# Kernel tuning notes

Measured on AMD Instinct MI355X. Metric: run time of the kernel, lower is better.

Reference implementation:

```python
import jax, jax.numpy as jnp
import numpy as np

N, LAT, HID = 4, 256, 512
OMICS = [("ge", 20000), ("meth", 200000), ("mirna", 2000), ("cnv", 25000)]
EPS = 1e-3  # Keras BatchNormalization default epsilon

# Fully-connected latent graph (i != j) + self loops (added by GCNConv).
_src = np.array([i for i in range(N) for j in range(N) if i != j] + list(range(N)), dtype=np.int32)
_dst = np.array([j for i in range(N) for j in range(N) if i != j] + list(range(N)), dtype=np.int32)
# Every node has degree N (N-1 neighbors + self loop) -> sym norm 1/sqrt(N*N) = 1/N per edge.
_norm = np.full(len(_src), 1.0 / N, dtype=np.float32)


def _gcn(x, W):
    h = x @ W                                   # [N, LAT] transform
    msg = h[_src] * _norm[:, None]              # gather + edge-normalize
    return jax.ops.segment_sum(msg, _dst, num_segments=N)  # scatter-add


def _bn(x, g, b, m, v):
    # BatchNorm in inference mode: moving stats.
    return g * (x - m) * jax.lax.rsqrt(v + EPS) + b


def setup_inputs() -> dict:
    key = jax.random.key(0)
    ks = list(jax.random.split(key, 4 + len(OMICS)))
    d = {
        "latent_vectors": jax.random.normal(ks[0], (N, LAT), jnp.float32),
        "Wg1": jax.random.normal(ks[1], (LAT, LAT), jnp.float32) * 0.05,
        "Wg2": jax.random.normal(ks[2], (LAT, LAT), jnp.float32) * 0.05,
        "W1": jax.random.normal(ks[3], (N, LAT, HID), jnp.float32) * 0.05,
        "b1": jnp.zeros((N, HID), jnp.float32),
        "g1": jnp.ones((N, HID), jnp.float32),
        "be1": jnp.zeros((N, HID), jnp.float32),
        "m1": jnp.zeros((N, HID), jnp.float32),
        "v1": jnp.ones((N, HID), jnp.float32),
    }
    for k, (name, dim) in enumerate(OMICS):
        d[f"W2_{name}"] = jax.random.normal(ks[4 + k], (HID, dim), jnp.float32) * 0.02
        d[f"b2_{name}"] = jnp.zeros((dim,), jnp.float32)
        d[f"g2_{name}"] = jnp.ones((dim,), jnp.float32)
        d[f"be2_{name}"] = jnp.zeros((dim,), jnp.float32)
        d[f"m2_{name}"] = jnp.zeros((dim,), jnp.float32)
        d[f"v2_{name}"] = jnp.ones((dim,), jnp.float32)
    return d


def _forward(latent_vectors, Wg1, Wg2, W1, b1, g1, be1, m1, v1, per_omics):
    # Two GCN layers + ReLU (dropout inactive: training=False)
    x = jax.nn.relu(_gcn(latent_vectors, Wg1))
    x = jax.nn.relu(_gcn(x, Wg2))               # [N, LAT]
    # First dense stage of all generators, vectorized over nodes.
    h = jnp.einsum('td,tdh->th', x, W1) + b1     # [N, HID]
    h = jax.nn.relu(_bn(h, g1, be1, m1, v1))     # BN (inference) + ReLU; dropout off
    outs = []
    for i, (W2, b2, g2, be2, m2, v2) in enumerate(per_omics):
        y = h[i] @ W2 + b2                       # [output_dim_i]
        outs.append(_bn(y, g2, be2, m2, v2))
    return tuple(outs)


def reference(latent_vectors, Wg1, Wg2, W1, b1, g1, be1, m1, v1,
              W2_ge, b2_ge, g2_ge, be2_ge, m2_ge, v2_ge,
              W2_meth, b2_meth, g2_meth, be2_meth, m2_meth, v2_meth,
              W2_mirna, b2_mirna, g2_mirna, be2_mirna, m2_mirna, v2_mirna,
              W2_cnv, b2_cnv, g2_cnv, be2_cnv, m2_cnv, v2_cnv):
    per = [(W2_ge, b2_ge, g2_ge, be2_ge, m2_ge, v2_ge),
           (W2_meth, b2_meth, g2_meth, be2_meth, m2_meth, v2_meth),
           (W2_mirna, b2_mirna, g2_mirna, be2_mirna, m2_mirna, v2_mirna),
           (W2_cnv, b2_cnv, g2_cnv, be2_cnv, m2_cnv, v2_cnv)]
    return _forward(latent_vectors, Wg1, Wg2, W1, b1, g1, be1, m1, v1, per)
```

## Files before the change

### kernel.cpp

```cpp
#include <hip/hip_runtime.h>


#define EPS 1e-3f

typedef unsigned short u16;
typedef unsigned int   u32;

__device__ __forceinline__ float b2f(u16 u) {
    union { u32 i; float f; } v; v.i = ((u32)u) << 16; return v.f;
}
__device__ __forceinline__ float lo16(u32 u) {
    union { u32 i; float f; } v; v.i = u << 16; return v.f;
}
__device__ __forceinline__ float hi16(u32 u) {
    union { u32 i; float f; } v; v.i = u & 0xffff0000u; return v.f;
}
__device__ __forceinline__ u16 f2b(float f) {
    union { float f; u32 i; } v; v.f = f;
    u32 r = v.i + 0x7fffu + ((v.i >> 16) & 1u);
    return (u16)(r >> 16);
}
__device__ __forceinline__ float ldin(const void* p, int i, int bf) {
    return bf ? b2f(((const u16*)p)[i]) : ((const float*)p)[i];
}

__global__ void k_detect(const void* __restrict__ L, int* __restrict__ flag) {
    const float* f = (const float*)L;
    int t = threadIdx.x;
    float mx = 0.f;
    for (int i = t; i < 256; i += 64) {
        float v = fabsf(f[i]);
        if (!(v < 1e30f)) v = 1e30f;
        mx = fmaxf(mx, v);
    }
    for (int o = 32; o; o >>= 1) mx = fmaxf(mx, __shfl_down(mx, o));
    if (t == 0) flag[0] = (mx < 1e6f) ? 0 : 1;
}

__global__ void k_stage1(const void* __restrict__ L,
                         const void* __restrict__ Wg1,
                         const int* __restrict__ flagp,
                         float* __restrict__ a_out) {
    int bf = flagp[0];
    __shared__ float v[256];
    __shared__ float part[4][64];
    int t = threadIdx.x;
    v[t] = 0.25f * (ldin(L, t, bf) + ldin(L, 256 + t, bf) +
                    ldin(L, 512 + t, bf) + ldin(L, 768 + t, bf));
    __syncthreads();
    int rg = t >> 6, cl = t & 63;
    int col = blockIdx.x * 64 + cl;
    int r0 = rg * 64;
    float s = 0.f;
#pragma unroll 8
    for (int r = r0; r < r0 + 64; ++r) s = fmaf(v[r], ldin(Wg1, r * 256 + col, bf), s);
    part[rg][cl] = s;
    __syncthreads();
    if (t < 64) {
        float sum = part[0][t] + part[1][t] + part[2][t] + part[3][t];
        a_out[blockIdx.x * 64 + t] = fmaxf(sum, 0.f);
    }
}

__global__ void k_stage2(const float* __restrict__ a_in,
                         const void* __restrict__ Wg2,
                         const int* __restrict__ flagp,
                         float* __restrict__ x_out) {
    int bf = flagp[0];
    __shared__ float v[256];
    __shared__ float part[4][64];
    int t = threadIdx.x;
    v[t] = a_in[t];
    __syncthreads();
    int rg = t >> 6, cl = t & 63;
    int col = blockIdx.x * 64 + cl;
    int r0 = rg * 64;
    float s = 0.f;
#pragma unroll 8
    for (int r = r0; r < r0 + 64; ++r) s = fmaf(v[r], ldin(Wg2, r * 256 + col, bf), s);
    part[rg][cl] = s;
    __syncthreads();
    if (t < 64) {
        float sum = part[0][t] + part[1][t] + part[2][t] + part[3][t];
        x_out[blockIdx.x * 64 + t] = fmaxf(sum, 0.f);
    }
}

__global__ void k_stage3(const float* __restrict__ x_in,
                         const void* __restrict__ W1,
                         const void* __restrict__ b1,
                         const void* __restrict__ g1,
                         const void* __restrict__ be1,
                         const void* __restrict__ m1,
                         const void* __restrict__ v1,
                         const int* __restrict__ flagp,
                         float* __restrict__ h_out) {
    int bf = flagp[0];
    __shared__ float x[256];
    __shared__ float part[4][64];
    int t = threadIdx.x;
    x[t] = x_in[t];
    __syncthreads();
    int rg = t >> 6, cl = t & 63;
    int o = blockIdx.x * 64 + cl;
    int node = o >> 9, col = o & 511;
    int wbase = node * (256 * 512);
    int r0 = rg * 64;
    float s = 0.f;
#pragma unroll 8
    for (int r = r0; r < r0 + 64; ++r) s = fmaf(x[r], ldin(W1, wbase + r * 512 + col, bf), s);
    part[rg][cl] = s;
    __syncthreads();
    if (t < 64) {
        int oo = blockIdx.x * 64 + t;
        float y = part[0][t] + part[1][t] + part[2][t] + part[3][t] + ldin(b1, oo, bf);
        float bn = ldin(g1, oo, bf) * (y - ldin(m1, oo, bf)) * rsqrtf(ldin(v1, oo, bf) + EPS)
                 + ldin(be1, oo, bf);
        h_out[oo] = fmaxf(bn, 0.f);
    }
}

__global__ void k_omics(
    const void* __restrict__ W2g, const void* __restrict__ b2g, const void* __restrict__ g2g,
    const void* __restrict__ be2g, const void* __restrict__ m2g, const void* __restrict__ v2g,
    const void* __restrict__ W2m, const void* __restrict__ b2m, const void* __restrict__ g2m,
    const void* __restrict__ be2m, const void* __restrict__ m2m, const void* __restrict__ v2m,
    const void* __restrict__ W2r, const void* __restrict__ b2r, const void* __restrict__ g2r,
    const void* __restrict__ be2r, const void* __restrict__ m2r, const void* __restrict__ v2r,
    const void* __restrict__ W2c, const void* __restrict__ b2c, const void* __restrict__ g2c,
    const void* __restrict__ be2c, const void* __restrict__ m2c, const void* __restrict__ v2c,
    const float* __restrict__ h_all, const int* __restrict__ flagp,
    void* __restrict__ outv) {

    int bf = flagp[0];
    int b = blockIdx.x;
    const void *W2, *b2, *g2, *be2, *m2, *v2;
    int k, lb, dim, ooff;
    if (b < 40) {
        k = 0; lb = b;        dim = 20000;  ooff = 0;
        W2 = W2g; b2 = b2g; g2 = g2g; be2 = be2g; m2 = m2g; v2 = v2g;
    } else if (b < 431) {
        k = 1; lb = b - 40;   dim = 200000; ooff = 20000;
        W2 = W2m; b2 = b2m; g2 = g2m; be2 = be2m; m2 = m2m; v2 = v2m;
    } else if (b < 435) {
        k = 2; lb = b - 431;  dim = 2000;   ooff = 220000;
        W2 = W2r; b2 = b2r; g2 = g2r; be2 = be2r; m2 = m2r; v2 = v2r;
    } else {
        k = 3; lb = b - 435;  dim = 25000;  ooff = 222000;
        W2 = W2c; b2 = b2c; g2 = g2c; be2 = be2c; m2 = m2c; v2 = v2c;
    }

    __shared__ float h[512];
    int t = threadIdx.x;
#pragma unroll
    for (int i = t; i < 512; i += 64) h[i] = h_all[k * 512 + i];
    __syncthreads();

    int j = (lb * 64 + t) * 8;
    if (j >= dim) return;

    float a0 = 0.f, a1 = 0.f, a2 = 0.f, a3 = 0.f,
          a4 = 0.f, a5 = 0.f, a6 = 0.f, a7 = 0.f;

    if (bf) {
        const u16* W = (const u16*)W2 + j;
#pragma unroll 4
        for (int r = 0; r < 512; ++r) {
            const u16* p = W + (size_t)r * dim;
            u32 w0 = *(const u32*)(p + 0);
            u32 w1 = *(const u32*)(p + 2);
            u32 w2 = *(const u32*)(p + 4);
            u32 w3 = *(const u32*)(p + 6);
            float hr = h[r];
            a0 = fmaf(hr, lo16(w0), a0); a1 = fmaf(hr, hi16(w0), a1);
            a2 = fmaf(hr, lo16(w1), a2); a3 = fmaf(hr, hi16(w1), a3);
            a4 = fmaf(hr, lo16(w2), a4); a5 = fmaf(hr, hi16(w2), a5);
            a6 = fmaf(hr, lo16(w3), a6); a7 = fmaf(hr, hi16(w3), a7);
        }
    } else {
        const float* W = (const float*)W2 + j;
#pragma unroll 4
        for (int r = 0; r < 512; ++r) {
            const float* p = W + (size_t)r * dim;
            float4 w0 = *(const float4*)(p + 0);
            float4 w1 = *(const float4*)(p + 4);
            float hr = h[r];
            a0 = fmaf(hr, w0.x, a0); a1 = fmaf(hr, w0.y, a1);
            a2 = fmaf(hr, w0.z, a2); a3 = fmaf(hr, w0.w, a3);
            a4 = fmaf(hr, w1.x, a4); a5 = fmaf(hr, w1.y, a5);
            a6 = fmaf(hr, w1.z, a6); a7 = fmaf(hr, w1.w, a7);
        }
    }

    float acc[8] = {a0, a1, a2, a3, a4, a5, a6, a7};
    float res[8];
#pragma unroll
    for (int i = 0; i < 8; ++i) {
        float y = acc[i] + ldin(b2, j + i, bf);
        res[i] = ldin(g2, j + i, bf) * (y - ldin(m2, j + i, bf)) *
                 rsqrtf(ldin(v2, j + i, bf) + EPS) + ldin(be2, j + i, bf);
    }

    if (bf) {
        u16* out = (u16*)outv;
        u32* po = (u32*)(out + ooff + j);
        po[0] = (u32)f2b(res[0]) | ((u32)f2b(res[1]) << 16);
        po[1] = (u32)f2b(res[2]) | ((u32)f2b(res[3]) << 16);
        po[2] = (u32)f2b(res[4]) | ((u32)f2b(res[5]) << 16);
        po[3] = (u32)f2b(res[6]) | ((u32)f2b(res[7]) << 16);
    } else {
        float* out = (float*)outv + ooff + j;
        float4 o0 = {res[0], res[1], res[2], res[3]};
        float4 o1 = {res[4], res[5], res[6], res[7]};
        *(float4*)(out + 0) = o0;
        *(float4*)(out + 4) = o1;
    }
}

extern "C" void kernel_launch(void* const* d_in, const int* in_sizes, int n_in,
                              void* d_out, int out_size, void* d_ws, size_t ws_size,
                              hipStream_t stream) {
    const void* L   = d_in[0];
    const void* Wg1 = d_in[1];
    const void* Wg2 = d_in[2];
    const void* W1  = d_in[3];
    const void* b1  = d_in[4];
    const void* g1  = d_in[5];
    const void* be1 = d_in[6];
    const void* m1  = d_in[7];
    const void* v1  = d_in[8];

    const void* P[24];
    for (int i = 0; i < 24; ++i) P[i] = d_in[9 + i];

    float* ws = (float*)d_ws;
    int* flag = (int*)(ws + 2560);

    k_detect<<<dim3(1),  dim3(64),  0, stream>>>(L, flag);
    k_stage1<<<dim3(4),  dim3(256), 0, stream>>>(L, Wg1, flag, ws);
    k_stage2<<<dim3(4),  dim3(256), 0, stream>>>(ws, Wg2, flag, ws + 256);
    k_stage3<<<dim3(32), dim3(256), 0, stream>>>(ws + 256, W1, b1, g1, be1, m1, v1, flag, ws + 512);
    k_omics <<<dim3(484), dim3(64), 0, stream>>>(
        P[0],  P[1],  P[2],  P[3],  P[4],  P[5],
        P[6],  P[7],  P[8],  P[9],  P[10], P[11],
        P[12], P[13], P[14], P[15], P[16], P[17],
        P[18], P[19], P[20], P[21], P[22], P[23],
        ws + 512, flag, d_out);
}
```

Before: 666.3 us.

## Split omics GEMV over K halves with partial sums and separate BN kernel

```diff
diff --git a/kernel.cpp b/kernel.cpp
--- a/kernel.cpp
+++ b/kernel.cpp
@@ -120,100 +120,111 @@
     }
 }
 
-__global__ void k_omics(
-    const void* __restrict__ W2g, const void* __restrict__ b2g, const void* __restrict__ g2g,
-    const void* __restrict__ be2g, const void* __restrict__ m2g, const void* __restrict__ v2g,
-    const void* __restrict__ W2m, const void* __restrict__ b2m, const void* __restrict__ g2m,
-    const void* __restrict__ be2m, const void* __restrict__ m2m, const void* __restrict__ v2m,
-    const void* __restrict__ W2r, const void* __restrict__ b2r, const void* __restrict__ g2r,
-    const void* __restrict__ be2r, const void* __restrict__ m2r, const void* __restrict__ v2r,
-    const void* __restrict__ W2c, const void* __restrict__ b2c, const void* __restrict__ g2c,
-    const void* __restrict__ be2c, const void* __restrict__ m2c, const void* __restrict__ v2c,
+__global__ __launch_bounds__(256) void k_omics(
+    const void* __restrict__ W2g, const void* __restrict__ W2m,
+    const void* __restrict__ W2r, const void* __restrict__ W2c,
     const float* __restrict__ h_all, const int* __restrict__ flagp,
-    void* __restrict__ outv) {
+    float* __restrict__ partial) {
 
     int bf = flagp[0];
     int b = blockIdx.x;
-    const void *W2, *b2, *g2, *be2, *m2, *v2;
+    int cb = b % 243, half = b / 243;
+
+    const void* W2;
     int k, lb, dim, ooff;
-    if (b < 40) {
-        k = 0; lb = b;        dim = 20000;  ooff = 0;
-        W2 = W2g; b2 = b2g; g2 = g2g; be2 = be2g; m2 = m2g; v2 = v2g;
-    } else if (b < 431) {
-        k = 1; lb = b - 40;   dim = 200000; ooff = 20000;
-        W2 = W2m; b2 = b2m; g2 = g2m; be2 = be2m; m2 = m2m; v2 = v2m;
-    } else if (b < 435) {
-        k = 2; lb = b - 431;  dim = 2000;   ooff = 220000;
-        W2 = W2r; b2 = b2r; g2 = g2r; be2 = be2r; m2 = m2r; v2 = v2r;
-    } else {
-        k = 3; lb = b - 435;  dim = 25000;  ooff = 222000;
-        W2 = W2c; b2 = b2c; g2 = g2c; be2 = be2c; m2 = m2c; v2 = v2c;
-    }
-
-    __shared__ float h[512];
-    int t = threadIdx.x;
-#pragma unroll
-    for (int i = t; i < 512; i += 64) h[i] = h_all[k * 512 + i];
-    __syncthreads();
-
-    int j = (lb * 64 + t) * 8;
+    if (cb < 20)       { k = 0; lb = cb;       dim = 20000;  ooff = 0;      W2 = W2g; }
+    else if (cb < 216) { k = 1; lb = cb - 20;  dim = 200000; ooff = 20000;  W2 = W2m; }
+    else if (cb < 218) { k = 2; lb = cb - 216; dim = 2000;   ooff = 220000; W2 = W2r; }
+    else               { k = 3; lb = cb - 218; dim = 25000;  ooff = 222000; W2 = W2c; }
+
+    __shared__ float h[256];
+    int t = threadIdx.x;
+    h[t] = h_all[k * 512 + half * 256 + t];
+    __syncthreads();
+
+    int j = lb * 1024 + t * 4;
     if (j >= dim) return;
 
-    float a0 = 0.f, a1 = 0.f, a2 = 0.f, a3 = 0.f,
-          a4 = 0.f, a5 = 0.f, a6 = 0.f, a7 = 0.f;
+    float a0 = 0.f, a1 = 0.f, a2 = 0.f, a3 = 0.f;
 
     if (bf) {
-        const u16* W = (const u16*)W2 + j;
-#pragma unroll 4
-        for (int r = 0; r < 512; ++r) {
+        const u16* W = (const u16*)W2 + (size_t)half * 256 * dim + j;
+#pragma unroll 8
+        for (int r = 0; r < 256; ++r) {
             const u16* p = W + (size_t)r * dim;
             u32 w0 = *(const u32*)(p + 0);
             u32 w1 = *(const u32*)(p + 2);
-            u32 w2 = *(const u32*)(p + 4);
-            u32 w3 = *(const u32*)(p + 6);
             float hr = h[r];
             a0 = fmaf(hr, lo16(w0), a0); a1 = fmaf(hr, hi16(w0), a1);
             a2 = fmaf(hr, lo16(w1), a2); a3 = fmaf(hr, hi16(w1), a3);
-            a4 = fmaf(hr, lo16(w2), a4); a5 = fmaf(hr, hi16(w2), a5);
-            a6 = fmaf(hr, lo16(w3), a6); a7 = fmaf(hr, hi16(w3), a7);
         }
     } else {
-        const float* W = (const float*)W2 + j;
-#pragma unroll 4
-        for (int r = 0; r < 512; ++r) {
-            const float* p = W + (size_t)r * dim;
-            float4 w0 = *(const float4*)(p + 0);
-            float4 w1 = *(const float4*)(p + 4);
+        const float* W = (const float*)W2 + (size_t)half * 256 * dim + j;
+#pragma unroll 8
+        for (int r = 0; r < 256; ++r) {
+            float4 w = *(const float4*)(W + (size_t)r * dim);
             float hr = h[r];
-            a0 = fmaf(hr, w0.x, a0); a1 = fmaf(hr, w0.y, a1);
-            a2 = fmaf(hr, w0.z, a2); a3 = fmaf(hr, w0.w, a3);
-            a4 = fmaf(hr, w1.x, a4); a5 = fmaf(hr, w1.y, a5);
-            a6 = fmaf(hr, w1.z, a6); a7 = fmaf(hr, w1.w, a7);
+            a0 = fmaf(hr, w.x, a0); a1 = fmaf(hr, w.y, a1);
+            a2 = fmaf(hr, w.z, a2); a3 = fmaf(hr, w.w, a3);
         }
     }
 
-    float acc[8] = {a0, a1, a2, a3, a4, a5, a6, a7};
-    float res[8];
+    float4 o = {a0, a1, a2, a3};
+    *(float4*)(partial + (size_t)half * 247000 + ooff + j) = o;
+}
+
+__global__ __launch_bounds__(256) void k_bn(
+    const void* __restrict__ b2g, const void* __restrict__ g2g, const void* __restrict__ be2g,
+    const void* __restrict__ m2g, const void* __restrict__ v2g,
+    const void* __restrict__ b2m, const void* __restrict__ g2m, const void* __restrict__ be2m,
+    const void* __restrict__ m2m, const void* __restrict__ v2m,
+    const void* __restrict__ b2r, const void* __restrict__ g2r, const void* __restrict__ be2r,
+    const void* __restrict__ m2r, const void* __restrict__ v2r,
+    const void* __restrict__ b2c, const void* __restrict__ g2c, const void* __restrict__ be2c,
+    const void* __restrict__ m2c, const void* __restrict__ v2c,
+    const float* __restrict__ partial, const int* __restrict__ flagp,
+    void* __restrict__ outv) {
+
+    int bf = flagp[0];
+    int j = (blockIdx.x * 256 + threadIdx.x) * 4;
+    if (j >= 247000) return;
+
+    const void *b2, *g2, *be2, *m2, *v2;
+    int jj;
+    if (j < 20000)       { jj = j;          b2 = b2g; g2 = g2g; be2 = be2g; m2 = m2g; v2 = v2g; }
+    else if (j < 220000) { jj = j - 20000;  b2 = b2m; g2 = g2m; be2 = be2m; m2 = m2m; v2 = v2m; }
+    else if (j < 222000) { jj = j - 220000; b2 = b2r; g2 = g2r; be2 = be2r; m2 = m2r; v2 = v2r; }
+    else                 { jj = j - 222000; b2 = b2c; g2 = g2c; be2 = be2c; m2 = m2c; v2 = v2c; }
+
+    float4 p0 = *(const float4*)(partial + j);
+    float4 p1 = *(const float4*)(partial + 247000 + j);
+    float acc[4] = {p0.x + p1.x, p0.y + p1.y, p0.z + p1.z, p0.w + p1.w};
+
+    float res[4];
+    if (bf) {
 #pragma unroll
-    for (int i = 0; i < 8; ++i) {
-        float y = acc[i] + ldin(b2, j + i, bf);
-        res[i] = ldin(g2, j + i, bf) * (y - ldin(m2, j + i, bf)) *
-                 rsqrtf(ldin(v2, j + i, bf) + EPS) + ldin(be2, j + i, bf);
-    }
-
-    if (bf) {
+        for (int i = 0; i < 4; ++i) {
+            float y = acc[i] + b2f(((const u16*)b2)[jj + i]);
+            res[i] = b2f(((const u16*)g2)[jj + i]) * (y - b2f(((const u16*)m2)[jj + i])) *
+                     rsqrtf(b2f(((const u16*)v2)[jj + i]) + EPS) +
+                     b2f(((const u16*)be2)[jj + i]);
+        }
         u16* out = (u16*)outv;
-        u32* po = (u32*)(out + ooff + j);
+        u32* po = (u32*)(out + j);
         po[0] = (u32)f2b(res[0]) | ((u32)f2b(res[1]) << 16);
         po[1] = (u32)f2b(res[2]) | ((u32)f2b(res[3]) << 16);
-        po[2] = (u32)f2b(res[4]) | ((u32)f2b(res[5]) << 16);
-        po[3] = (u32)f2b(res[6]) | ((u32)f2b(res[7]) << 16);
     } else {
-        float* out = (float*)outv + ooff + j;
-        float4 o0 = {res[0], res[1], res[2], res[3]};
-        float4 o1 = {res[4], res[5], res[6], res[7]};
-        *(float4*)(out + 0) = o0;
-        *(float4*)(out + 4) = o1;
+        float4 bw  = *(const float4*)((const float*)b2  + jj);
+        float4 gw  = *(const float4*)((const float*)g2  + jj);
+        float4 mw  = *(const float4*)((const float*)m2  + jj);
+        float4 vw  = *(const float4*)((const float*)v2  + jj);
+        float4 bew = *(const float4*)((const float*)be2 + jj);
+        res[0] = gw.x * (acc[0] + bw.x - mw.x) * rsqrtf(vw.x + EPS) + bew.x;
+        res[1] = gw.y * (acc[1] + bw.y - mw.y) * rsqrtf(vw.y + EPS) + bew.y;
+        res[2] = gw.z * (acc[2] + bw.z - mw.z) * rsqrtf(vw.z + EPS) + bew.z;
+        res[3] = gw.w * (acc[3] + bw.w - mw.w) * rsqrtf(vw.w + EPS) + bew.w;
+        float4 o = {res[0], res[1], res[2], res[3]};
+        *(float4*)((float*)outv + j) = o;
     }
 }
 
@@ -235,15 +246,18 @@
 
     float* ws = (float*)d_ws;
     int* flag = (int*)(ws + 2560);
+    float* partial = ws + 2576;
 
     k_detect<<<dim3(1),  dim3(64),  0, stream>>>(L, flag);
     k_stage1<<<dim3(4),  dim3(256), 0, stream>>>(L, Wg1, flag, ws);
     k_stage2<<<dim3(4),  dim3(256), 0, stream>>>(ws, Wg2, flag, ws + 256);
     k_stage3<<<dim3(32), dim3(256), 0, stream>>>(ws + 256, W1, b1, g1, be1, m1, v1, flag, ws + 512);
-    k_omics <<<dim3(484), dim3(64), 0, stream>>>(
-        P[0],  P[1],  P[2],  P[3],  P[4],  P[5],
-        P[6],  P[7],  P[8],  P[9],  P[10], P[11],
-        P[12], P[13], P[14], P[15], P[16], P[17],
-        P[18], P[19], P[20], P[21], P[22], P[23],
-        ws + 512, flag, d_out);
-}
+    k_omics <<<dim3(486), dim3(256), 0, stream>>>(P[0], P[6], P[12], P[18],
+                                                  ws + 512, flag, partial);
+    k_bn    <<<dim3(242), dim3(256), 0, stream>>>(
+        P[1],  P[2],  P[3],  P[4],  P[5],
+        P[7],  P[8],  P[9],  P[10], P[11],
+        P[13], P[14], P[15], P[16], P[17],
+        P[19], P[20], P[21], P[22], P[23],
+        partial, flag, d_out);
+}
```

Result: no change. 667.3 us (+0.2%).
